# Performance work log

Hardware: AMD Instinct MI355X
Metric: run time of the kernel (lower is better)

The kernel has to match this reference:

```python
import jax, jax.numpy as jnp
import numpy as np

N, NFEAT, NHID = 10000, 128, 64


def _gc(x, adj, W, b):
    # GraphConvolution: adj @ (x @ W) + b
    return adj @ (x @ W) + b


def _fwd(x, adj, Wg0, bg0, Wg1, bg1, Wt0, bt0, Wt1, bt1,
         W000, b000, W001, b001, W100, b100, W101, b101,
         Wo0, bo0, Wo1, bo1, Wpp, bpp, Wpp2, bpp2, a, t):
    H = Wg0.shape[1]
    # outcome GCN stack (n_in=2), dropout is eval no-op
    rep_o = jax.nn.relu(_gc(x, adj, Wg0, bg0))
    rep_o = jax.nn.relu(_gc(rep_o, adj, Wg1, bg1))
    # treatment GCN stack
    rep_t = jax.nn.relu(_gc(x, adj, Wt0, bt0))
    rep_t = jax.nn.relu(_gc(rep_t, adj, Wt1, bt1))

    rep_cat = jnp.concatenate([rep_o, rep_t], axis=1)  # [N, 2H]
    # edge score(i,j) = [rep_cat_i ; rep_cat_j] @ a  =  s_src_i + s_dst_j
    s_src = rep_cat @ a[:2 * H, 0]   # [N]
    s_dst = rep_cat @ a[2 * H:, 0]   # [N]
    scores = s_src[:, None] + s_dst[None, :]          # [N, N]
    # only nonzero adj entries get a score; rest remain 0 (index_put into zeros)
    att = jnp.where(adj != 0, scores, jnp.zeros((), scores.dtype))
    att = jax.nn.softmax(att, axis=1)                 # full dense row softmax

    rep_out = att @ rep_t + rep_o                     # [N, H]

    treatment = jax.nn.sigmoid((rep_t @ Wpp + bpp) @ Wpp2 + bpp2)  # [N, 2]

    rep0 = rep_out
    rep1 = rep_out
    y00 = jax.nn.relu(rep0 @ W000 + b000)
    y10 = jax.nn.relu(rep1 @ W100 + b100)
    y00 = jax.nn.relu(y00 @ W001 + b001)
    y10 = jax.nn.relu(y10 @ W101 + b101)
    y0 = (y00 @ Wo0 + bo0).reshape(-1)
    y1 = (y10 @ Wo1 + bo1).reshape(-1)
    y = jnp.where(t > 0, y1, y0)
    return (y, rep_out, treatment)


def setup_inputs() -> dict:
    key = jax.random.key(0)
    ks = jax.random.split(key, 32)
    H = NHID
    x = jax.random.normal(ks[0], (N, NFEAT), dtype=jnp.float32)
    u = jax.random.uniform(ks[1], (N, N), dtype=jnp.float32)
    adj = jnp.where(u < 0.002, u, jnp.zeros((), jnp.float32))
    t = jax.random.randint(ks[2], (N,), 0, 2, dtype=jnp.int32)

    def lin(k, fi, fo):
        s = 1.0 / np.sqrt(fi)
        kw, kb = jax.random.split(k)
        return (jax.random.uniform(kw, (fi, fo), jnp.float32, -s, s),
                jax.random.uniform(kb, (fo,), jnp.float32, -s, s))

    Wg0, bg0 = lin(ks[3], NFEAT, H)
    Wg1, bg1 = lin(ks[4], H, H)
    Wt0, bt0 = lin(ks[5], NFEAT, H)
    Wt1, bt1 = lin(ks[6], H, H)
    W000, b000 = lin(ks[7], H, H)
    W001, b001 = lin(ks[8], H, H)
    W100, b100 = lin(ks[9], H, H)
    W101, b101 = lin(ks[10], H, H)
    Wo0, bo0 = lin(ks[11], H, 1)
    Wo1, bo1 = lin(ks[12], H, 1)
    Wpp, bpp = lin(ks[13], H, H)
    Wpp2, bpp2 = lin(ks[14], H, 2)
    # torch init is xavier with gain=0 (all zeros); use small random for a
    # meaningful correctness baseline
    a = jax.random.normal(ks[15], (4 * H, 1), dtype=jnp.float32) * 0.1
    return dict(x=x, adj=adj, t=t,
                Wg0=Wg0, bg0=bg0, Wg1=Wg1, bg1=bg1,
                Wt0=Wt0, bt0=bt0, Wt1=Wt1, bt1=bt1,
                W000=W000, b000=b000, W001=W001, b001=b001,
                W100=W100, b100=b100, W101=W101, b101=b101,
                Wo0=Wo0, bo0=bo0, Wo1=Wo1, bo1=bo1,
                Wpp=Wpp, bpp=bpp, Wpp2=Wpp2, bpp2=bpp2, a=a)


def reference(x, adj, t, Wg0, bg0, Wg1, bg1, Wt0, bt0, Wt1, bt1,
              W000, b000, W001, b001, W100, b100, W101, b101,
              Wo0, bo0, Wo1, bo1, Wpp, bpp, Wpp2, bpp2, a):
    return _fwd(x, adj, Wg0, bg0, Wg1, bg1, Wt0, bt0, Wt1, bt1,
                W000, b000, W001, b001, W100, b100, W101, b101,
                Wo0, bo0, Wo1, bo1, Wpp, bpp, Wpp2, bpp2, a, t)
```

## Files before the change

kernel.cpp:

```cpp
#include <hip/hip_runtime.h>
#include <hip/hip_bf16.h>

#define N_NODES 10000
#define CAP 64

#define OFF_CNT     0
#define OFF_COLSUM  10000
#define OFF_COLS    10064
#define OFF_VALS    650064
#define OFF_SSRC    1290064
#define OFF_SDST    1300064
#define OFF_P       1310064
#define OFF_Q       1950064
#define OFF_R1      2590064
#define OFF_T1      3230064
#define OFF_U       3870064
#define OFF_V       4510064


__global__ void zero_kernel(int* p, int n) {
    int i = blockIdx.x * blockDim.x + threadIdx.x;
    if (i < n) p[i] = 0;
}

__global__ void sparsify_kernel(const float4* __restrict__ adj4,
                                int* __restrict__ cnt,
                                int* __restrict__ cols,
                                float* __restrict__ vals) {
    const int row = blockIdx.y;
    const int row4 = N_NODES / 4;
    int base = blockIdx.x * 1024 + threadIdx.x;
    #pragma unroll
    for (int it = 0; it < 4; ++it) {
        int idx = base + it * 256;
        if (idx < row4) {
            float4 v = adj4[(size_t)row * row4 + idx];
            float vv[4] = {v.x, v.y, v.z, v.w};
            #pragma unroll
            for (int l = 0; l < 4; ++l) {
                if (vv[l] != 0.0f) {
                    int pos = atomicAdd(&cnt[row], 1);
                    if (pos < CAP) {
                        cols[(size_t)row * CAP + pos] = idx * 4 + l;
                        vals[(size_t)row * CAP + pos] = vv[l];
                    }
                }
            }
        }
    }
}

__global__ void gemm128_kernel(const float* __restrict__ x,
                               const float* __restrict__ W,
                               float* __restrict__ out) {
    __shared__ float Ws[128 * 64];
    __shared__ float xs[4 * 128];
    int tid = threadIdx.x;
    for (int i = tid; i < 128 * 64; i += 256) Ws[i] = W[i];
    int row0 = blockIdx.x * 4;
    for (int i = tid; i < 4 * 128; i += 256)
        xs[i] = x[(size_t)row0 * 128 + i];
    __syncthreads();
    int r = tid >> 6, f = tid & 63;
    float acc = 0.0f;
    #pragma unroll 8
    for (int k = 0; k < 128; ++k) acc += xs[r * 128 + k] * Ws[k * 64 + f];
    out[(size_t)(row0 + r) * 64 + f] = acc;
}

__global__ void gemm64_kernel(const float* __restrict__ in,
                              const float* __restrict__ W,
                              const float* __restrict__ b,
                              float* __restrict__ out,
                              int relu_flag) {
    __shared__ float Ws[64 * 64];
    __shared__ float xs[4 * 64];
    int tid = threadIdx.x;
    for (int i = tid; i < 64 * 64; i += 256) Ws[i] = W[i];
    int row0 = blockIdx.x * 4;
    xs[tid] = in[(size_t)row0 * 64 + tid];
    __syncthreads();
    int r = tid >> 6, f = tid & 63;
    float acc = b ? b[f] : 0.0f;
    #pragma unroll
    for (int k = 0; k < 64; ++k) acc += xs[r * 64 + k] * Ws[k * 64 + f];
    if (relu_flag) acc = fmaxf(acc, 0.0f);
    out[(size_t)(row0 + r) * 64 + f] = acc;
}

__global__ void spmm_kernel(const int* __restrict__ cnt,
                            const int* __restrict__ cols,
                            const float* __restrict__ vals,
                            const float* __restrict__ in,
                            const float* __restrict__ b,
                            float* __restrict__ out) {
    int tid = threadIdx.x;
    int row = blockIdx.x * 4 + (tid >> 6);
    int f = tid & 63;
    int c = min(cnt[row], CAP);
    const int* cp = cols + (size_t)row * CAP;
    const float* vp = vals + (size_t)row * CAP;
    float acc = 0.0f;
    for (int p = 0; p < c; ++p)
        acc += vp[p] * in[(size_t)cp[p] * 64 + f];
    acc += b[f];
    out[(size_t)row * 64 + f] = fmaxf(acc, 0.0f);
}

__global__ void score_kernel(const float* __restrict__ ro,
                             const float* __restrict__ rt,
                             const float* __restrict__ a,
                             float* __restrict__ s_src,
                             float* __restrict__ s_dst) {
    int tid = threadIdx.x;
    int row = blockIdx.x * 4 + (tid >> 6);
    int f = tid & 63;
    float vo = ro[(size_t)row * 64 + f], vt = rt[(size_t)row * 64 + f];
    float ps = vo * a[f] + vt * a[64 + f];
    float pd = vo * a[128 + f] + vt * a[192 + f];
    #pragma unroll
    for (int off = 32; off >= 1; off >>= 1) {
        ps += __shfl_xor(ps, off, 64);
        pd += __shfl_xor(pd, off, 64);
    }
    if (f == 0) { s_src[row] = ps; s_dst[row] = pd; }
}

__global__ void colsum_kernel(const float* __restrict__ rt, float* __restrict__ colsum) {
    int tid = threadIdx.x;
    int f = tid & 63, w = tid >> 6;
    int start = blockIdx.x * 250;
    float acc = 0.0f;
    for (int i = start + w; i < start + 250; i += 4)
        acc += rt[(size_t)i * 64 + f];
    atomicAdd(&colsum[f], acc);
}

__global__ void attn_kernel(const int* __restrict__ cnt,
                            const int* __restrict__ cols,
                            const float* __restrict__ s_src,
                            const float* __restrict__ s_dst,
                            const float* __restrict__ colsum,
                            const float* __restrict__ ro,
                            const float* __restrict__ rt,
                            float* __restrict__ rep_out) {
    int tid = threadIdx.x;
    int row = blockIdx.x * 4 + (tid >> 6);
    int lane = tid & 63;
    int c = min(cnt[row], CAP);
    const int* cp = cols + (size_t)row * CAP;
    float ssrc = s_src[row];
    float s_l = -1e30f;
    if (lane < c) s_l = ssrc + s_dst[cp[lane]];
    float m = s_l;
    #pragma unroll
    for (int off = 32; off >= 1; off >>= 1) m = fmaxf(m, __shfl_xor(m, off, 64));
    m = fmaxf(m, 0.0f);
    float e_l = (lane < c) ? expf(s_l - m) : 0.0f;
    float Z = e_l;
    #pragma unroll
    for (int off = 32; off >= 1; off >>= 1) Z += __shfl_xor(Z, off, 64);
    float em = expf(-m);
    Z += (float)(N_NODES - c) * em;
    float acc = 0.0f;
    for (int p = 0; p < c; ++p) {
        float ep = __shfl(e_l, p, 64);
        int colp = cp[p];
        acc += (ep - em) * rt[(size_t)colp * 64 + lane];
    }
    float outv = (acc + em * colsum[lane]) / Z + ro[(size_t)row * 64 + lane];
    rep_out[(size_t)row * 64 + lane] = outv;
}

__global__ void treat_kernel(const float* __restrict__ h,
                             const float* __restrict__ Wpp2,
                             const float* __restrict__ bpp2,
                             float* __restrict__ out_treat) {
    int tid = threadIdx.x;
    int row = blockIdx.x * 4 + (tid >> 6);
    int k = tid & 63;
    float hv = h[(size_t)row * 64 + k];
    float p0 = hv * Wpp2[k * 2 + 0];
    float p1 = hv * Wpp2[k * 2 + 1];
    #pragma unroll
    for (int off = 32; off >= 1; off >>= 1) {
        p0 += __shfl_xor(p0, off, 64);
        p1 += __shfl_xor(p1, off, 64);
    }
    if (k == 0) {
        out_treat[(size_t)row * 2 + 0] = 1.0f / (1.0f + expf(-(p0 + bpp2[0])));
        out_treat[(size_t)row * 2 + 1] = 1.0f / (1.0f + expf(-(p1 + bpp2[1])));
    }
}

__global__ void y_kernel(const float* __restrict__ h0, const float* __restrict__ h1,
                         const float* __restrict__ Wo0, const float* __restrict__ bo0,
                         const float* __restrict__ Wo1, const float* __restrict__ bo1,
                         const int* __restrict__ t, float* __restrict__ y) {
    int tid = threadIdx.x;
    int row = blockIdx.x * 4 + (tid >> 6);
    int k = tid & 63;
    float p0 = h0[(size_t)row * 64 + k] * Wo0[k];
    float p1 = h1[(size_t)row * 64 + k] * Wo1[k];
    #pragma unroll
    for (int off = 32; off >= 1; off >>= 1) {
        p0 += __shfl_xor(p0, off, 64);
        p1 += __shfl_xor(p1, off, 64);
    }
    if (k == 0) {
        float y0 = p0 + bo0[0];
        float y1 = p1 + bo1[0];
        y[row] = (t[row] > 0) ? y1 : y0;
    }
}


extern "C" void kernel_launch(void* const* d_in, const int* in_sizes, int n_in,
                              void* d_out, int out_size, void* d_ws, size_t ws_size,
                              hipStream_t stream) {
    const float* x    = (const float*)d_in[0];
    const float* adj  = (const float*)d_in[1];
    const int*   t    = (const int*)d_in[2];
    const float* Wg0  = (const float*)d_in[3];
    const float* bg0  = (const float*)d_in[4];
    const float* Wg1  = (const float*)d_in[5];
    const float* bg1  = (const float*)d_in[6];
    const float* Wt0  = (const float*)d_in[7];
    const float* bt0  = (const float*)d_in[8];
    const float* Wt1  = (const float*)d_in[9];
    const float* bt1  = (const float*)d_in[10];
    const float* W000 = (const float*)d_in[11];
    const float* b000 = (const float*)d_in[12];
    const float* W001 = (const float*)d_in[13];
    const float* b001 = (const float*)d_in[14];
    const float* W100 = (const float*)d_in[15];
    const float* b100 = (const float*)d_in[16];
    const float* W101 = (const float*)d_in[17];
    const float* b101 = (const float*)d_in[18];
    const float* Wo0  = (const float*)d_in[19];
    const float* bo0  = (const float*)d_in[20];
    const float* Wo1  = (const float*)d_in[21];
    const float* bo1  = (const float*)d_in[22];
    const float* Wpp  = (const float*)d_in[23];
    const float* bpp  = (const float*)d_in[24];
    const float* Wpp2 = (const float*)d_in[25];
    const float* bpp2 = (const float*)d_in[26];
    const float* a    = (const float*)d_in[27];

    float* ws = (float*)d_ws;
    int*   cnt    = (int*)(ws + OFF_CNT);
    float* colsum = ws + OFF_COLSUM;
    int*   cols   = (int*)(ws + OFF_COLS);
    float* vals   = ws + OFF_VALS;
    float* s_src  = ws + OFF_SSRC;
    float* s_dst  = ws + OFF_SDST;
    float* P      = ws + OFF_P;
    float* Q      = ws + OFF_Q;
    float* R1     = ws + OFF_R1;
    float* T1     = ws + OFF_T1;
    float* U      = ws + OFF_U;
    float* V      = ws + OFF_V;

    float* out_y    = (float*)d_out;
    float* rep_out  = (float*)d_out + N_NODES;
    float* out_trt  = (float*)d_out + N_NODES + N_NODES * 64;

    const int RB = N_NODES / 4;

    zero_kernel<<<(10064 + 255) / 256, 256, 0, stream>>>((int*)d_ws, 10064);

    sparsify_kernel<<<dim3(3, N_NODES), 256, 0, stream>>>((const float4*)adj, cnt, cols, vals);

    gemm128_kernel<<<RB, 256, 0, stream>>>(x, Wg0, P);
    gemm128_kernel<<<RB, 256, 0, stream>>>(x, Wt0, Q);
    spmm_kernel<<<RB, 256, 0, stream>>>(cnt, cols, vals, P, bg0, R1);
    spmm_kernel<<<RB, 256, 0, stream>>>(cnt, cols, vals, Q, bt0, T1);

    gemm64_kernel<<<RB, 256, 0, stream>>>(R1, Wg1, nullptr, P, 0);
    gemm64_kernel<<<RB, 256, 0, stream>>>(T1, Wt1, nullptr, Q, 0);
    spmm_kernel<<<RB, 256, 0, stream>>>(cnt, cols, vals, P, bg1, R1);
    spmm_kernel<<<RB, 256, 0, stream>>>(cnt, cols, vals, Q, bt1, T1);

    score_kernel<<<RB, 256, 0, stream>>>(R1, T1, a, s_src, s_dst);
    colsum_kernel<<<40, 256, 0, stream>>>(T1, colsum);

    attn_kernel<<<RB, 256, 0, stream>>>(cnt, cols, s_src, s_dst, colsum, R1, T1, rep_out);

    gemm64_kernel<<<RB, 256, 0, stream>>>(T1, Wpp, bpp, P, 0);
    treat_kernel<<<RB, 256, 0, stream>>>(P, Wpp2, bpp2, out_trt);

    gemm64_kernel<<<RB, 256, 0, stream>>>(rep_out, W000, b000, U, 1);
    gemm64_kernel<<<RB, 256, 0, stream>>>(U, W001, b001, V, 1);
    gemm64_kernel<<<RB, 256, 0, stream>>>(rep_out, W100, b100, U, 1);
    gemm64_kernel<<<RB, 256, 0, stream>>>(U, W101, b101, P, 1);

    y_kernel<<<RB, 256, 0, stream>>>(V, P, Wo0, bo0, Wo1, bo1, t, out_y);
}
```

Before: 806.0 us.

## Fuse GCN pipeline into five kernels with 8-row blocks

Collapses roughly twenty launches into five fused kernels. Sparsification now also zeroes the counters and column sums, the two first-layer GEMMs share one x tile, each aggregation is fused with the following dense GEMM or the score/colsum/treatment heads, and attention is fused with both MLP heads and the y output. Blocks process 8 rows instead of 4 so each weight load into LDS is reused across more rows. This removes launch overhead and intermediate global round trips, but puts more LDS per block and launches fewer, heavier blocks, which may lower occupancy. The sparsify kernel now walks 4 full rows per block, which changes how the dominant 400MB adjacency read is spread across blocks.

```diff
diff --git a/kernel.cpp b/kernel.cpp
--- a/kernel.cpp
+++ b/kernel.cpp
@@ -2,7 +2,8 @@
 #include <hip/hip_bf16.h>
 
 #define N_NODES 10000
-#define CAP 64
+#define ROW4    2500
+#define CAP     64
 
 #define OFF_CNT     0
 #define OFF_COLSUM  10000
@@ -10,31 +11,38 @@
 #define OFF_VALS    650064
 #define OFF_SSRC    1290064
 #define OFF_SDST    1300064
-#define OFF_P       1310064
-#define OFF_Q       1950064
-#define OFF_R1      2590064
-#define OFF_T1      3230064
-#define OFF_U       3870064
-#define OFF_V       4510064
-
-
-__global__ void zero_kernel(int* p, int n) {
-    int i = blockIdx.x * blockDim.x + threadIdx.x;
-    if (i < n) p[i] = 0;
-}
-
-__global__ void sparsify_kernel(const float4* __restrict__ adj4,
-                                int* __restrict__ cnt,
-                                int* __restrict__ cols,
-                                float* __restrict__ vals) {
-    const int row = blockIdx.y;
-    const int row4 = N_NODES / 4;
-    int base = blockIdx.x * 1024 + threadIdx.x;
-    #pragma unroll
-    for (int it = 0; it < 4; ++it) {
-        int idx = base + it * 256;
-        if (idx < row4) {
-            float4 v = adj4[(size_t)row * row4 + idx];
+#define OFF_B1      1310064
+#define OFF_B2      1950064
+#define OFF_B3      2590064
+#define OFF_B4      3230064
+
+__device__ __forceinline__ float wave_sum(float v) {
+    #pragma unroll
+    for (int off = 32; off >= 1; off >>= 1) v += __shfl_xor(v, off, 64);
+    return v;
+}
+__device__ __forceinline__ float wave_max(float v) {
+    #pragma unroll
+    for (int off = 32; off >= 1; off >>= 1) v = fmaxf(v, __shfl_xor(v, off, 64));
+    return v;
+}
+
+__global__ void k1_sparsify(const float4* __restrict__ adj4,
+                            int* __restrict__ cnt,
+                            int* __restrict__ cols,
+                            float* __restrict__ vals,
+                            float* __restrict__ colsum) {
+    int tid = threadIdx.x;
+    int row0 = blockIdx.x * 4;
+    if (tid < 4) cnt[row0 + tid] = 0;
+    if (blockIdx.x == 0 && tid < 64) colsum[tid] = 0.0f;
+    __syncthreads();
+    #pragma unroll
+    for (int r = 0; r < 4; ++r) {
+        int row = row0 + r;
+        const float4* rp = adj4 + (size_t)row * ROW4;
+        for (int idx = tid; idx < ROW4; idx += 256) {
+            float4 v = rp[idx];
             float vv[4] = {v.x, v.y, v.z, v.w};
             #pragma unroll
             for (int l = 0; l < 4; ++l) {
@@ -50,167 +58,252 @@
     }
 }
 
-__global__ void gemm128_kernel(const float* __restrict__ x,
-                               const float* __restrict__ W,
-                               float* __restrict__ out) {
+__global__ void k2_gemm128(const float* __restrict__ x,
+                           const float* __restrict__ Wg0,
+                           const float* __restrict__ Wt0,
+                           float* __restrict__ P, float* __restrict__ Q) {
     __shared__ float Ws[128 * 64];
-    __shared__ float xs[4 * 128];
+    __shared__ float xs[8 * 128];
     int tid = threadIdx.x;
-    for (int i = tid; i < 128 * 64; i += 256) Ws[i] = W[i];
-    int row0 = blockIdx.x * 4;
-    for (int i = tid; i < 4 * 128; i += 256)
-        xs[i] = x[(size_t)row0 * 128 + i];
-    __syncthreads();
-    int r = tid >> 6, f = tid & 63;
-    float acc = 0.0f;
-    #pragma unroll 8
-    for (int k = 0; k < 128; ++k) acc += xs[r * 128 + k] * Ws[k * 64 + f];
-    out[(size_t)(row0 + r) * 64 + f] = acc;
-}
-
-__global__ void gemm64_kernel(const float* __restrict__ in,
-                              const float* __restrict__ W,
-                              const float* __restrict__ b,
-                              float* __restrict__ out,
-                              int relu_flag) {
-    __shared__ float Ws[64 * 64];
-    __shared__ float xs[4 * 64];
-    int tid = threadIdx.x;
-    for (int i = tid; i < 64 * 64; i += 256) Ws[i] = W[i];
-    int row0 = blockIdx.x * 4;
-    xs[tid] = in[(size_t)row0 * 64 + tid];
-    __syncthreads();
-    int r = tid >> 6, f = tid & 63;
-    float acc = b ? b[f] : 0.0f;
-    #pragma unroll
-    for (int k = 0; k < 64; ++k) acc += xs[r * 64 + k] * Ws[k * 64 + f];
-    if (relu_flag) acc = fmaxf(acc, 0.0f);
-    out[(size_t)(row0 + r) * 64 + f] = acc;
-}
-
-__global__ void spmm_kernel(const int* __restrict__ cnt,
-                            const int* __restrict__ cols,
+    int row0 = blockIdx.x * 8;
+    ((float4*)xs)[tid] = ((const float4*)(x + (size_t)row0 * 128))[tid];
+    for (int i = tid; i < 2048; i += 256) ((float4*)Ws)[i] = ((const float4*)Wg0)[i];
+    __syncthreads();
+    int sub = tid >> 6, f = tid & 63;
+    float accP[2];
+    #pragma unroll
+    for (int g = 0; g < 2; ++g) {
+        const float* xr = xs + (g * 4 + sub) * 128;
+        float acc = 0.0f;
+        #pragma unroll 8
+        for (int k = 0; k < 128; k += 4) {
+            float4 xv = *(const float4*)(xr + k);
+            acc += xv.x * Ws[(k + 0) * 64 + f] + xv.y * Ws[(k + 1) * 64 + f]
+                 + xv.z * Ws[(k + 2) * 64 + f] + xv.w * Ws[(k + 3) * 64 + f];
+        }
+        accP[g] = acc;
+    }
+    #pragma unroll
+    for (int g = 0; g < 2; ++g)
+        P[(size_t)(row0 + g * 4 + sub) * 64 + f] = accP[g];
+    __syncthreads();
+    for (int i = tid; i < 2048; i += 256) ((float4*)Ws)[i] = ((const float4*)Wt0)[i];
+    __syncthreads();
+    #pragma unroll
+    for (int g = 0; g < 2; ++g) {
+        const float* xr = xs + (g * 4 + sub) * 128;
+        float acc = 0.0f;
+        #pragma unroll 8
+        for (int k = 0; k < 128; k += 4) {
+            float4 xv = *(const float4*)(xr + k);
+            acc += xv.x * Ws[(k + 0) * 64 + f] + xv.y * Ws[(k + 1) * 64 + f]
+                 + xv.z * Ws[(k + 2) * 64 + f] + xv.w * Ws[(k + 3) * 64 + f];
+        }
+        Q[(size_t)(row0 + g * 4 + sub) * 64 + f] = acc;
+    }
+}
+
+__global__ void k3_agg_gemm(const int* __restrict__ cnt, const int* __restrict__ cols,
                             const float* __restrict__ vals,
-                            const float* __restrict__ in,
-                            const float* __restrict__ b,
-                            float* __restrict__ out) {
-    int tid = threadIdx.x;
-    int row = blockIdx.x * 4 + (tid >> 6);
-    int f = tid & 63;
-    int c = min(cnt[row], CAP);
-    const int* cp = cols + (size_t)row * CAP;
-    const float* vp = vals + (size_t)row * CAP;
-    float acc = 0.0f;
-    for (int p = 0; p < c; ++p)
-        acc += vp[p] * in[(size_t)cp[p] * 64 + f];
-    acc += b[f];
-    out[(size_t)row * 64 + f] = fmaxf(acc, 0.0f);
-}
-
-__global__ void score_kernel(const float* __restrict__ ro,
-                             const float* __restrict__ rt,
+                            const float* __restrict__ P, const float* __restrict__ Q,
+                            const float* __restrict__ bg0, const float* __restrict__ bt0,
+                            const float* __restrict__ Wg1, const float* __restrict__ Wt1,
+                            float* __restrict__ P2, float* __restrict__ Q2) {
+    __shared__ float Wa[64 * 64], Wb[64 * 64];
+    __shared__ float ra[8 * 64], rb[8 * 64];
+    int tid = threadIdx.x, row0 = blockIdx.x * 8, sub = tid >> 6, f = tid & 63;
+    for (int i = tid; i < 1024; i += 256) {
+        ((float4*)Wa)[i] = ((const float4*)Wg1)[i];
+        ((float4*)Wb)[i] = ((const float4*)Wt1)[i];
+    }
+    float bo = bg0[f], bt = bt0[f];
+    #pragma unroll
+    for (int g = 0; g < 2; ++g) {
+        int lr = g * 4 + sub, row = row0 + lr;
+        int c = min(cnt[row], CAP);
+        const int* cp = cols + (size_t)row * CAP;
+        const float* vp = vals + (size_t)row * CAP;
+        float aP = 0.0f, aQ = 0.0f;
+        for (int p = 0; p < c; ++p) {
+            int col = cp[p]; float v = vp[p];
+            aP += v * P[(size_t)col * 64 + f];
+            aQ += v * Q[(size_t)col * 64 + f];
+        }
+        ra[lr * 64 + f] = fmaxf(aP + bo, 0.0f);
+        rb[lr * 64 + f] = fmaxf(aQ + bt, 0.0f);
+    }
+    __syncthreads();
+    #pragma unroll
+    for (int g = 0; g < 2; ++g) {
+        int lr = g * 4 + sub, row = row0 + lr;
+        const float* rra = ra + lr * 64;
+        const float* rrb = rb + lr * 64;
+        float aA = 0.0f, aB = 0.0f;
+        #pragma unroll 8
+        for (int k = 0; k < 64; k += 4) {
+            float4 va = *(const float4*)(rra + k);
+            float4 vb = *(const float4*)(rrb + k);
+            aA += va.x * Wa[(k + 0) * 64 + f] + va.y * Wa[(k + 1) * 64 + f]
+                + va.z * Wa[(k + 2) * 64 + f] + va.w * Wa[(k + 3) * 64 + f];
+            aB += vb.x * Wb[(k + 0) * 64 + f] + vb.y * Wb[(k + 1) * 64 + f]
+                + vb.z * Wb[(k + 2) * 64 + f] + vb.w * Wb[(k + 3) * 64 + f];
+        }
+        P2[(size_t)row * 64 + f] = aA;
+        Q2[(size_t)row * 64 + f] = aB;
+    }
+}
+
+__global__ void k4_agg_score(const int* __restrict__ cnt, const int* __restrict__ cols,
+                             const float* __restrict__ vals,
+                             const float* __restrict__ P2, const float* __restrict__ Q2,
+                             const float* __restrict__ bg1, const float* __restrict__ bt1,
                              const float* __restrict__ a,
-                             float* __restrict__ s_src,
-                             float* __restrict__ s_dst) {
-    int tid = threadIdx.x;
-    int row = blockIdx.x * 4 + (tid >> 6);
-    int f = tid & 63;
-    float vo = ro[(size_t)row * 64 + f], vt = rt[(size_t)row * 64 + f];
-    float ps = vo * a[f] + vt * a[64 + f];
-    float pd = vo * a[128 + f] + vt * a[192 + f];
-    #pragma unroll
-    for (int off = 32; off >= 1; off >>= 1) {
-        ps += __shfl_xor(ps, off, 64);
-        pd += __shfl_xor(pd, off, 64);
-    }
-    if (f == 0) { s_src[row] = ps; s_dst[row] = pd; }
-}
-
-__global__ void colsum_kernel(const float* __restrict__ rt, float* __restrict__ colsum) {
-    int tid = threadIdx.x;
-    int f = tid & 63, w = tid >> 6;
-    int start = blockIdx.x * 250;
-    float acc = 0.0f;
-    for (int i = start + w; i < start + 250; i += 4)
-        acc += rt[(size_t)i * 64 + f];
-    atomicAdd(&colsum[f], acc);
-}
-
-__global__ void attn_kernel(const int* __restrict__ cnt,
-                            const int* __restrict__ cols,
-                            const float* __restrict__ s_src,
-                            const float* __restrict__ s_dst,
-                            const float* __restrict__ colsum,
-                            const float* __restrict__ ro,
-                            const float* __restrict__ rt,
-                            float* __restrict__ rep_out) {
-    int tid = threadIdx.x;
-    int row = blockIdx.x * 4 + (tid >> 6);
-    int lane = tid & 63;
-    int c = min(cnt[row], CAP);
-    const int* cp = cols + (size_t)row * CAP;
-    float ssrc = s_src[row];
-    float s_l = -1e30f;
-    if (lane < c) s_l = ssrc + s_dst[cp[lane]];
-    float m = s_l;
-    #pragma unroll
-    for (int off = 32; off >= 1; off >>= 1) m = fmaxf(m, __shfl_xor(m, off, 64));
-    m = fmaxf(m, 0.0f);
-    float e_l = (lane < c) ? expf(s_l - m) : 0.0f;
-    float Z = e_l;
-    #pragma unroll
-    for (int off = 32; off >= 1; off >>= 1) Z += __shfl_xor(Z, off, 64);
-    float em = expf(-m);
-    Z += (float)(N_NODES - c) * em;
-    float acc = 0.0f;
-    for (int p = 0; p < c; ++p) {
-        float ep = __shfl(e_l, p, 64);
-        int colp = cp[p];
-        acc += (ep - em) * rt[(size_t)colp * 64 + lane];
-    }
-    float outv = (acc + em * colsum[lane]) / Z + ro[(size_t)row * 64 + lane];
-    rep_out[(size_t)row * 64 + lane] = outv;
-}
-
-__global__ void treat_kernel(const float* __restrict__ h,
-                             const float* __restrict__ Wpp2,
-                             const float* __restrict__ bpp2,
-                             float* __restrict__ out_treat) {
-    int tid = threadIdx.x;
-    int row = blockIdx.x * 4 + (tid >> 6);
-    int k = tid & 63;
-    float hv = h[(size_t)row * 64 + k];
-    float p0 = hv * Wpp2[k * 2 + 0];
-    float p1 = hv * Wpp2[k * 2 + 1];
-    #pragma unroll
-    for (int off = 32; off >= 1; off >>= 1) {
-        p0 += __shfl_xor(p0, off, 64);
-        p1 += __shfl_xor(p1, off, 64);
-    }
-    if (k == 0) {
-        out_treat[(size_t)row * 2 + 0] = 1.0f / (1.0f + expf(-(p0 + bpp2[0])));
-        out_treat[(size_t)row * 2 + 1] = 1.0f / (1.0f + expf(-(p1 + bpp2[1])));
-    }
-}
-
-__global__ void y_kernel(const float* __restrict__ h0, const float* __restrict__ h1,
-                         const float* __restrict__ Wo0, const float* __restrict__ bo0,
-                         const float* __restrict__ Wo1, const float* __restrict__ bo1,
-                         const int* __restrict__ t, float* __restrict__ y) {
-    int tid = threadIdx.x;
-    int row = blockIdx.x * 4 + (tid >> 6);
-    int k = tid & 63;
-    float p0 = h0[(size_t)row * 64 + k] * Wo0[k];
-    float p1 = h1[(size_t)row * 64 + k] * Wo1[k];
-    #pragma unroll
-    for (int off = 32; off >= 1; off >>= 1) {
-        p0 += __shfl_xor(p0, off, 64);
-        p1 += __shfl_xor(p1, off, 64);
-    }
-    if (k == 0) {
-        float y0 = p0 + bo0[0];
-        float y1 = p1 + bo1[0];
-        y[row] = (t[row] > 0) ? y1 : y0;
+                             const float* __restrict__ Wpp, const float* __restrict__ bpp,
+                             const float* __restrict__ Wpp2, const float* __restrict__ bpp2,
+                             float* __restrict__ rep_o, float* __restrict__ rep_t,
+                             float* __restrict__ s_src, float* __restrict__ s_dst,
+                             float* __restrict__ colsum, float* __restrict__ out_trt) {
+    __shared__ float Wp[64 * 64];
+    __shared__ float rts[8 * 64];
+    int tid = threadIdx.x, row0 = blockIdx.x * 8, sub = tid >> 6, f = tid & 63;
+    for (int i = tid; i < 1024; i += 256) ((float4*)Wp)[i] = ((const float4*)Wpp)[i];
+    float bo = bg1[f], bt = bt1[f];
+    float a0 = a[f], a1 = a[64 + f], a2 = a[128 + f], a3 = a[192 + f];
+    #pragma unroll
+    for (int g = 0; g < 2; ++g) {
+        int lr = g * 4 + sub, row = row0 + lr;
+        int c = min(cnt[row], CAP);
+        const int* cp = cols + (size_t)row * CAP;
+        const float* vp = vals + (size_t)row * CAP;
+        float aO = 0.0f, aT = 0.0f;
+        for (int p = 0; p < c; ++p) {
+            int col = cp[p]; float v = vp[p];
+            aO += v * P2[(size_t)col * 64 + f];
+            aT += v * Q2[(size_t)col * 64 + f];
+        }
+        float vo = fmaxf(aO + bo, 0.0f);
+        float vt = fmaxf(aT + bt, 0.0f);
+        rep_o[(size_t)row * 64 + f] = vo;
+        rep_t[(size_t)row * 64 + f] = vt;
+        rts[lr * 64 + f] = vt;
+        float ps = wave_sum(vo * a0 + vt * a1);
+        float pd = wave_sum(vo * a2 + vt * a3);
+        if (f == 0) { s_src[row] = ps; s_dst[row] = pd; }
+    }
+    __syncthreads();
+    if (sub == 0) {
+        float cs = 0.0f;
+        #pragma unroll
+        for (int lr = 0; lr < 8; ++lr) cs += rts[lr * 64 + f];
+        atomicAdd(&colsum[f], cs);
+    }
+    float bp = bpp[f], w20 = Wpp2[f * 2 + 0], w21 = Wpp2[f * 2 + 1];
+    #pragma unroll
+    for (int g = 0; g < 2; ++g) {
+        int lr = g * 4 + sub, row = row0 + lr;
+        const float* rr = rts + lr * 64;
+        float u = bp;
+        #pragma unroll 8
+        for (int k = 0; k < 64; k += 4) {
+            float4 rv = *(const float4*)(rr + k);
+            u += rv.x * Wp[(k + 0) * 64 + f] + rv.y * Wp[(k + 1) * 64 + f]
+               + rv.z * Wp[(k + 2) * 64 + f] + rv.w * Wp[(k + 3) * 64 + f];
+        }
+        float p0 = wave_sum(u * w20);
+        float p1 = wave_sum(u * w21);
+        if (f == 0) {
+            out_trt[(size_t)row * 2 + 0] = 1.0f / (1.0f + expf(-(p0 + bpp2[0])));
+            out_trt[(size_t)row * 2 + 1] = 1.0f / (1.0f + expf(-(p1 + bpp2[1])));
+        }
+    }
+}
+
+__global__ void k5_attn_heads(const int* __restrict__ cnt, const int* __restrict__ cols,
+                              const float* __restrict__ s_src, const float* __restrict__ s_dst,
+                              const float* __restrict__ colsum,
+                              const float* __restrict__ rep_o, const float* __restrict__ rep_t,
+                              const float* __restrict__ W000, const float* __restrict__ b000,
+                              const float* __restrict__ W001, const float* __restrict__ b001,
+                              const float* __restrict__ W100, const float* __restrict__ b100,
+                              const float* __restrict__ W101, const float* __restrict__ b101,
+                              const float* __restrict__ Wo0, const float* __restrict__ bo0,
+                              const float* __restrict__ Wo1, const float* __restrict__ bo1,
+                              const int* __restrict__ t,
+                              float* __restrict__ out_y, float* __restrict__ out_rep) {
+    __shared__ float WA[64 * 64], WB[64 * 64];
+    __shared__ float reps[8 * 64], u0s[8 * 64], u1s[8 * 64];
+    int tid = threadIdx.x, row0 = blockIdx.x * 8, sub = tid >> 6, f = tid & 63;
+    for (int i = tid; i < 1024; i += 256) {
+        ((float4*)WA)[i] = ((const float4*)W000)[i];
+        ((float4*)WB)[i] = ((const float4*)W100)[i];
+    }
+    float csf = colsum[f];
+    #pragma unroll
+    for (int g = 0; g < 2; ++g) {
+        int lr = g * 4 + sub, row = row0 + lr;
+        int c = min(cnt[row], CAP);
+        const int* cp = cols + (size_t)row * CAP;
+        float ssrc = s_src[row];
+        int   col_l = (f < c) ? cp[f] : 0;
+        float s_l   = (f < c) ? ssrc + s_dst[col_l] : -1e30f;
+        float m = fmaxf(wave_max(s_l), 0.0f);
+        float e_l = (f < c) ? expf(s_l - m) : 0.0f;
+        float em = expf(-m);
+        float Z = wave_sum(e_l) + (float)(N_NODES - c) * em;
+        float acc = 0.0f;
+        for (int p = 0; p < c; ++p) {
+            float ep  = __shfl(e_l, p, 64);
+            int  colp = __shfl(col_l, p, 64);
+            acc += (ep - em) * rep_t[(size_t)colp * 64 + f];
+        }
+        float outv = (acc + em * csf) / Z + rep_o[(size_t)row * 64 + f];
+        out_rep[(size_t)row * 64 + f] = outv;
+        reps[lr * 64 + f] = outv;
+    }
+    __syncthreads();
+    float bA = b000[f], bB = b100[f];
+    #pragma unroll
+    for (int g = 0; g < 2; ++g) {
+        int lr = g * 4 + sub;
+        const float* rr = reps + lr * 64;
+        float u0 = bA, u1 = bB;
+        #pragma unroll 8
+        for (int k = 0; k < 64; k += 4) {
+            float4 rv = *(const float4*)(rr + k);
+            u0 += rv.x * WA[(k + 0) * 64 + f] + rv.y * WA[(k + 1) * 64 + f]
+                + rv.z * WA[(k + 2) * 64 + f] + rv.w * WA[(k + 3) * 64 + f];
+            u1 += rv.x * WB[(k + 0) * 64 + f] + rv.y * WB[(k + 1) * 64 + f]
+                + rv.z * WB[(k + 2) * 64 + f] + rv.w * WB[(k + 3) * 64 + f];
+        }
+        u0s[lr * 64 + f] = fmaxf(u0, 0.0f);
+        u1s[lr * 64 + f] = fmaxf(u1, 0.0f);
+    }
+    __syncthreads();
+    for (int i = tid; i < 1024; i += 256) {
+        ((float4*)WA)[i] = ((const float4*)W001)[i];
+        ((float4*)WB)[i] = ((const float4*)W101)[i];
+    }
+    __syncthreads();
+    float bC = b001[f], bD = b101[f], wo0 = Wo0[f], wo1 = Wo1[f];
+    #pragma unroll
+    for (int g = 0; g < 2; ++g) {
+        int lr = g * 4 + sub, row = row0 + lr;
+        const float* r0 = u0s + lr * 64;
+        const float* r1 = u1s + lr * 64;
+        float v0 = bC, v1 = bD;
+        #pragma unroll 8
+        for (int k = 0; k < 64; k += 4) {
+            float4 a0 = *(const float4*)(r0 + k);
+            float4 a1 = *(const float4*)(r1 + k);
+            v0 += a0.x * WA[(k + 0) * 64 + f] + a0.y * WA[(k + 1) * 64 + f]
+                + a0.z * WA[(k + 2) * 64 + f] + a0.w * WA[(k + 3) * 64 + f];
+            v1 += a1.x * WB[(k + 0) * 64 + f] + a1.y * WB[(k + 1) * 64 + f]
+                + a1.z * WB[(k + 2) * 64 + f] + a1.w * WB[(k + 3) * 64 + f];
+        }
+        float y0 = wave_sum(fmaxf(v0, 0.0f) * wo0);
+        float y1 = wave_sum(fmaxf(v1, 0.0f) * wo1);
+        if (f == 0)
+            out_y[row] = (t[row] > 0) ? (y1 + bo1[0]) : (y0 + bo0[0]);
     }
 }
 
@@ -254,45 +347,23 @@
     float* vals   = ws + OFF_VALS;
     float* s_src  = ws + OFF_SSRC;
     float* s_dst  = ws + OFF_SDST;
-    float* P      = ws + OFF_P;
-    float* Q      = ws + OFF_Q;
-    float* R1     = ws + OFF_R1;
-    float* T1     = ws + OFF_T1;
-    float* U      = ws + OFF_U;
-    float* V      = ws + OFF_V;
-
-    float* out_y    = (float*)d_out;
-    float* rep_out  = (float*)d_out + N_NODES;
-    float* out_trt  = (float*)d_out + N_NODES + N_NODES * 64;
-
-    const int RB = N_NODES / 4;
-
-    zero_kernel<<<(10064 + 255) / 256, 256, 0, stream>>>((int*)d_ws, 10064);
-
-    sparsify_kernel<<<dim3(3, N_NODES), 256, 0, stream>>>((const float4*)adj, cnt, cols, vals);
-
-    gemm128_kernel<<<RB, 256, 0, stream>>>(x, Wg0, P);
-    gemm128_kernel<<<RB, 256, 0, stream>>>(x, Wt0, Q);
-    spmm_kernel<<<RB, 256, 0, stream>>>(cnt, cols, vals, P, bg0, R1);
-    spmm_kernel<<<RB, 256, 0, stream>>>(cnt, cols, vals, Q, bt0, T1);
-
-    gemm64_kernel<<<RB, 256, 0, stream>>>(R1, Wg1, nullptr, P, 0);
-    gemm64_kernel<<<RB, 256, 0, stream>>>(T1, Wt1, nullptr, Q, 0);
-    spmm_kernel<<<RB, 256, 0, stream>>>(cnt, cols, vals, P, bg1, R1);
-    spmm_kernel<<<RB, 256, 0, stream>>>(cnt, cols, vals, Q, bt1, T1);
-
-    score_kernel<<<RB, 256, 0, stream>>>(R1, T1, a, s_src, s_dst);
-    colsum_kernel<<<40, 256, 0, stream>>>(T1, colsum);
-
-    attn_kernel<<<RB, 256, 0, stream>>>(cnt, cols, s_src, s_dst, colsum, R1, T1, rep_out);
-
-    gemm64_kernel<<<RB, 256, 0, stream>>>(T1, Wpp, bpp, P, 0);
-    treat_kernel<<<RB, 256, 0, stream>>>(P, Wpp2, bpp2, out_trt);
-
-    gemm64_kernel<<<RB, 256, 0, stream>>>(rep_out, W000, b000, U, 1);
-    gemm64_kernel<<<RB, 256, 0, stream>>>(U, W001, b001, V, 1);
-    gemm64_kernel<<<RB, 256, 0, stream>>>(rep_out, W100, b100, U, 1);
-    gemm64_kernel<<<RB, 256, 0, stream>>>(U, W101, b101, P, 1);
-
-    y_kernel<<<RB, 256, 0, stream>>>(V, P, Wo0, bo0, Wo1, bo1, t, out_y);
-}
+    float* B1     = ws + OFF_B1;
+    float* B2     = ws + OFF_B2;
+    float* B3     = ws + OFF_B3;
+    float* B4     = ws + OFF_B4;
+
+    float* out_y   = (float*)d_out;
+    float* out_rep = (float*)d_out + N_NODES;
+    float* out_trt = (float*)d_out + N_NODES + N_NODES * 64;
+
+    k1_sparsify<<<2500, 256, 0, stream>>>((const float4*)adj, cnt, cols, vals, colsum);
+    k2_gemm128<<<1250, 256, 0, stream>>>(x, Wg0, Wt0, B1, B2);
+    k3_agg_gemm<<<1250, 256, 0, stream>>>(cnt, cols, vals, B1, B2, bg0, bt0, Wg1, Wt1, B3, B4);
+    k4_agg_score<<<1250, 256, 0, stream>>>(cnt, cols, vals, B3, B4, bg1, bt1, a,
+                                           Wpp, bpp, Wpp2, bpp2,
+                                           B1, B2, s_src, s_dst, colsum, out_trt);
+    k5_attn_heads<<<1250, 256, 0, stream>>>(cnt, cols, s_src, s_dst, colsum, B1, B2,
+                                            W000, b000, W001, b001,
+                                            W100, b100, W101, b101,
+                                            Wo0, bo0, Wo1, bo1, t, out_y, out_rep);
+}
```

New measurement: 774.8 us. 3.9% less time.
